# Performance work log

Measured on AMD Instinct MI355X. Metric: run time of the kernel, lower is better.

The kernel has to match this reference:

```python
import jax, jax.numpy as jnp
import numpy as np

N_MODEL = 1024
N_HEADS = 16
KV_HEADS = 4
HEAD_DIM = N_MODEL // N_HEADS          # 64
KV_MODEL = HEAD_DIM * KV_HEADS         # 256
GROUPS = N_HEADS // KV_HEADS           # 4
B, S = 4, 2048


def _rmsnorm(x):
    return x * jax.lax.rsqrt(jnp.mean(x * x, axis=-1, keepdims=True) + 1e-6)


def _act_quant(x):
    # 8-bit absmax per-token quantization (BitNet b1.58)
    scale = 127.0 / jnp.clip(jnp.max(jnp.abs(x), axis=-1, keepdims=True), 1e-5)
    return jnp.clip(jnp.round(x * scale), -128.0, 127.0) / scale


def _weight_quant(w):
    # ternary absmean quantization
    scale = 1.0 / jnp.clip(jnp.mean(jnp.abs(w)), 1e-5)
    return jnp.clip(jnp.round(w * scale), -1.0, 1.0) / scale


def bitlinear(x, w, b):
    xn = _rmsnorm(x)
    xq = xn + jax.lax.stop_gradient(_act_quant(xn) - xn)   # STE
    wq = w + jax.lax.stop_gradient(_weight_quant(w) - w)   # STE
    return jnp.einsum('...i,oi->...o', xq, wq) + b


def setup_inputs() -> dict:
    key = jax.random.key(0)
    ks = jax.random.split(key, 11)
    sq = 1.0 / np.sqrt(N_MODEL)
    sk = 1.0 / np.sqrt(KV_MODEL)
    return {
        'query': jax.random.normal(ks[0], (B, S, N_MODEL), jnp.float32),
        'key':   jax.random.normal(ks[1], (B, S, N_MODEL), jnp.float32),
        'value': jax.random.normal(ks[2], (B, S, N_MODEL), jnp.float32),
        'Wq': jax.random.normal(ks[3], (N_MODEL, N_MODEL), jnp.float32) * sq,
        'bq': jnp.zeros((N_MODEL,), jnp.float32),
        'Wk': jax.random.normal(ks[4], (KV_MODEL, N_MODEL), jnp.float32) * sq,
        'bk': jnp.zeros((KV_MODEL,), jnp.float32),
        'Wv': jax.random.normal(ks[5], (KV_MODEL, N_MODEL), jnp.float32) * sq,
        'bv': jnp.zeros((KV_MODEL,), jnp.float32),
        'Wo': jax.random.normal(ks[6], (N_MODEL, KV_MODEL), jnp.float32) * sk,
        'bo': jnp.zeros((N_MODEL,), jnp.float32),
    }


def reference(query, key, value, Wq, bq, Wk, bk, Wv, bv, Wo, bo):
    b = query.shape[0]
    Q = bitlinear(query, Wq, bq)   # [b, n, n_model]
    K = bitlinear(key,   Wk, bk)   # [b, s, kv_model]
    V = bitlinear(value, Wv, bv)   # [b, s, kv_model]

    # [b, h, n, d] layouts
    Q = Q.reshape(b, -1, N_HEADS, HEAD_DIM).transpose(0, 2, 1, 3)
    K = K.reshape(b, -1, KV_HEADS, HEAD_DIM).transpose(0, 2, 1, 3)
    V = V.reshape(b, -1, KV_HEADS, HEAD_DIM).transpose(0, 2, 1, 3)

    # group query heads: [b, g, kv_h, n, d]
    Qg = Q.reshape(b, KV_HEADS, GROUPS, -1, HEAD_DIM).transpose(0, 2, 1, 3, 4)
    # NOTE: faithful to the module, the einsum output has no 'g' axis,
    # so the grouped query heads are SUMMED over g.
    energy = jnp.einsum('bghnd,bhsd->bhns', Qg, K)  # [b, kv_h, n, s]

    scale = jnp.sqrt(jnp.float32(HEAD_DIM))
    attention = jax.nn.softmax(energy / scale, axis=-1)
    x = jnp.einsum('bhns,bhsd->bhnd', attention, V)  # [b, kv_h, n, d]
    x = x.transpose(0, 2, 1, 3).reshape(b, -1, KV_MODEL)
    x = bitlinear(x, Wo, bo)       # [b, n, n_model]
    return (x, attention)
```

## Files before the change

### kernel.cpp

```cpp
#include <hip/hip_runtime.h>
#include <stdint.h>

#define N_MODELC 1024
#define KV_MODELC 256
#define BATCH 4
#define SEQ 2048
#define NTOK (BATCH*SEQ)

typedef __attribute__((ext_vector_type(4))) float f32x4;
typedef __attribute__((ext_vector_type(4))) int   i32x4;
typedef __attribute__((ext_vector_type(8))) short s16x8;
typedef __attribute__((ext_vector_type(4))) short s16x4;

#define LOG2E 1.4426950408889634f
#define PSHIFT 32.0f

__device__ __forceinline__ unsigned short f2bf(float f){
  unsigned u = __builtin_bit_cast(unsigned, f);
  u = (u + 0x7FFFu + ((u>>16)&1u)) >> 16;
  return (unsigned short)u;
}
__device__ __forceinline__ float bf2f(unsigned short b){
  return __builtin_bit_cast(float, ((unsigned)b)<<16);
}

__global__ __launch_bounds__(256) void k_actquant1024(
    const float* __restrict__ xq_in, const float* __restrict__ xk_in, const float* __restrict__ xv_in,
    int8_t* __restrict__ q8q, int8_t* __restrict__ q8k, int8_t* __restrict__ q8v,
    float* __restrict__ scq, float* __restrict__ sck, float* __restrict__ scv)
{
  int row = blockIdx.x, which = blockIdx.y, t = threadIdx.x;
  const float* x = (which==0)?xq_in:(which==1)?xk_in:xv_in;
  int8_t* q8 = (which==0)?q8q:(which==1)?q8k:q8v;
  float* sc = (which==0)?scq:(which==1)?sck:scv;
  const float* xr = x + (size_t)row*N_MODELC;
  float4 v = reinterpret_cast<const float4*>(xr)[t];
  float ss = v.x*v.x + v.y*v.y + v.z*v.z + v.w*v.w;
  float am = fmaxf(fmaxf(fabsf(v.x),fabsf(v.y)), fmaxf(fabsf(v.z),fabsf(v.w)));
  #pragma unroll
  for (int m=32;m;m>>=1){ ss += __shfl_xor(ss,m,64); am = fmaxf(am, __shfl_xor(am,m,64)); }
  __shared__ float red[8];
  int wid = t>>6;
  if ((t&63)==0){ red[wid]=ss; red[4+wid]=am; }
  __syncthreads();
  ss = red[0]+red[1]+red[2]+red[3];
  am = fmaxf(fmaxf(red[4],red[5]), fmaxf(red[6],red[7]));
  float rinv = rsqrtf(ss*(1.0f/N_MODELC) + 1e-6f);
  float clipv = fmaxf(am*rinv, 1e-5f);
  float qs = 127.0f/clipv;
  float fsc = rinv*qs;
  char4 o;
  o.x = (signed char)(int)fminf(127.f, fmaxf(-128.f, rintf(v.x*fsc)));
  o.y = (signed char)(int)fminf(127.f, fmaxf(-128.f, rintf(v.y*fsc)));
  o.z = (signed char)(int)fminf(127.f, fmaxf(-128.f, rintf(v.z*fsc)));
  o.w = (signed char)(int)fminf(127.f, fmaxf(-128.f, rintf(v.w*fsc)));
  reinterpret_cast<char4*>(q8 + (size_t)row*N_MODELC)[t] = o;
  if (t==0) sc[row] = clipv*(1.0f/127.0f);
}

__global__ __launch_bounds__(64) void k_actquant256(
    const float* __restrict__ X, int8_t* __restrict__ q8, float* __restrict__ sc)
{
  int row = blockIdx.x, l = threadIdx.x;
  float4 v = reinterpret_cast<const float4*>(X + (size_t)row*KV_MODELC)[l];
  float ss = v.x*v.x + v.y*v.y + v.z*v.z + v.w*v.w;
  float am = fmaxf(fmaxf(fabsf(v.x),fabsf(v.y)), fmaxf(fabsf(v.z),fabsf(v.w)));
  #pragma unroll
  for (int m=32;m;m>>=1){ ss += __shfl_xor(ss,m,64); am = fmaxf(am, __shfl_xor(am,m,64)); }
  float rinv = rsqrtf(ss*(1.0f/KV_MODELC) + 1e-6f);
  float clipv = fmaxf(am*rinv, 1e-5f);
  float qs = 127.0f/clipv;
  float fsc = rinv*qs;
  char4 o;
  o.x = (signed char)(int)fminf(127.f, fmaxf(-128.f, rintf(v.x*fsc)));
  o.y = (signed char)(int)fminf(127.f, fmaxf(-128.f, rintf(v.y*fsc)));
  o.z = (signed char)(int)fminf(127.f, fmaxf(-128.f, rintf(v.z*fsc)));
  o.w = (signed char)(int)fminf(127.f, fmaxf(-128.f, rintf(v.w*fsc)));
  reinterpret_cast<char4*>(q8 + (size_t)row*KV_MODELC)[l] = o;
  if (l==0) sc[row] = clipv*(1.0f/127.0f);
}

__global__ __launch_bounds__(256) void k_wabs_partial(
    const float* __restrict__ Wq, const float* __restrict__ Wk,
    const float* __restrict__ Wv, const float* __restrict__ Wo, float* __restrict__ partial)
{
  int mat = blockIdx.y;
  const float* w = (mat==0)?Wq:(mat==1)?Wk:(mat==2)?Wv:Wo;
  int n = (mat==0)?(N_MODELC*N_MODELC):(KV_MODELC*N_MODELC);
  float s = 0.f;
  for (int i = blockIdx.x*256 + threadIdx.x; i < n; i += 256*256) s += fabsf(w[i]);
  #pragma unroll
  for (int m=32;m;m>>=1) s += __shfl_xor(s,m,64);
  __shared__ float red[4];
  int wid = threadIdx.x>>6;
  if ((threadIdx.x&63)==0) red[wid]=s;
  __syncthreads();
  if (threadIdx.x==0) partial[mat*256 + blockIdx.x] = red[0]+red[1]+red[2]+red[3];
}

__global__ __launch_bounds__(256) void k_wfinal(const float* __restrict__ partial, float* __restrict__ wfac)
{
  int mat = blockIdx.x, t = threadIdx.x;
  float s = partial[mat*256 + t];
  #pragma unroll
  for (int m=32;m;m>>=1) s += __shfl_xor(s,m,64);
  __shared__ float red[4];
  int wid = t>>6;
  if ((t&63)==0) red[wid]=s;
  __syncthreads();
  if (t==0){
    float tot = red[0]+red[1]+red[2]+red[3];
    float n = (mat==0)?(float)(N_MODELC*N_MODELC):(float)(KV_MODELC*N_MODELC);
    wfac[mat] = fmaxf(tot/n, 1e-5f);
  }
}

__global__ __launch_bounds__(256) void k_tern(
    const float* __restrict__ Wq, const float* __restrict__ Wk,
    const float* __restrict__ Wv, const float* __restrict__ Wo,
    const float* __restrict__ wfac,
    int8_t* __restrict__ Wqs, int8_t* __restrict__ Wkt,
    int8_t* __restrict__ Wvt, int8_t* __restrict__ Wot)
{
  int mat = blockIdx.y;
  int idx = blockIdx.x*256 + threadIdx.x;
  if (mat==0){
    float s = 1.0f/wfac[0];
    int op = idx>>10, i = idx&1023;
    int kv = op>>6, d = op&63;
    int acc = 0;
    #pragma unroll
    for (int g=0; g<4; g++){
      float w = Wq[(size_t)(kv*256 + g*64 + d)*N_MODELC + i];
      float r = fminf(1.f, fmaxf(-1.f, rintf(w*s)));
      acc += (int)r;
    }
    Wqs[idx] = (int8_t)acc;
  } else {
    const float* w = (mat==1)?Wk:(mat==2)?Wv:Wo;
    int8_t* o = (mat==1)?Wkt:(mat==2)?Wvt:Wot;
    float s = 1.0f/wfac[mat];
    float r = fminf(1.f, fmaxf(-1.f, rintf(w[idx]*s)));
    o[idx] = (int8_t)r;
  }
}

template<int MODE>
__global__ __launch_bounds__(512) void k_gemm_i8_1024(
    const int8_t* __restrict__ A, const int8_t* __restrict__ B,
    const float* __restrict__ rowscale, const float* __restrict__ wfac, int wfi,
    const float* __restrict__ bias, unsigned short* __restrict__ outp)
{
  __shared__ i32x4 redk[4][4][64];
  __shared__ unsigned short tlds[(MODE==2)?64:1][72];
  const int KDIM = 1024;
  int mb = blockIdx.x*64, nb = blockIdx.y*64;
  int w = threadIdx.x>>6, l = threadIdx.x&63, lr = l&15, lk = l>>4;
  int rw = w&3, kh = w>>2;
  const int8_t* Ap = A + (size_t)(mb + rw*16 + lr)*KDIM + kh*512 + lk*16;
  const int8_t* Bp = B + (size_t)(nb + lr)*KDIM + kh*512 + lk*16;
  i32x4 acc[4];
  #pragma unroll
  for (int f=0; f<4; f++) acc[f] = i32x4{0,0,0,0};
  #pragma unroll 4
  for (int kk=0; kk<512; kk+=64){
    i32x4 a = *reinterpret_cast<const i32x4*>(Ap + kk);
    #pragma unroll
    for (int f=0; f<4; f++){
      i32x4 b = *reinterpret_cast<const i32x4*>(Bp + (size_t)f*16*KDIM + kk);
      acc[f] = __builtin_amdgcn_mfma_i32_16x16x64_i8(a, b, acc[f], 0, 0, 0);
    }
  }
  if (kh==1){
    #pragma unroll
    for (int f=0; f<4; f++) redk[rw][f][l] = acc[f];
  }
  __syncthreads();
  if (kh==0){
    float wf = wfac[wfi];
    #pragma unroll
    for (int f=0; f<4; f++){
      acc[f] += redk[rw][f][l];
      int col = nb + f*16 + lr;
      float bval;
      if constexpr (MODE==0){
        int kv = col>>6, d = col&63;
        const float* bb = bias + kv*256 + d;
        bval = bb[0]+bb[64]+bb[128]+bb[192];
      } else {
        bval = bias[col];
      }
      #pragma unroll
      for (int r=0; r<4; r++){
        int row = mb + rw*16 + lk*4 + r;
        float val = (float)acc[f][r] * (rowscale[row]*wf) + bval;
        if constexpr (MODE==0){
          int bb2 = row>>11, s = row&2047, kvh = col>>6, d = col&63;
          outp[(((size_t)(bb2*4+kvh))*SEQ + s)*64 + d] = f2bf(0.125f*val);
        } else if constexpr (MODE==1){
          int bb2 = row>>11, s = row&2047, kvh = col>>6, d = col&63;
          outp[(((size_t)(bb2*4+kvh))*SEQ + s)*64 + d] = f2bf(val);
        } else {
          tlds[f*16+lr][rw*16 + lk*4 + r] = f2bf(val);
        }
      }
    }
  }
  if constexpr (MODE==2){
    __syncthreads();
    int u = threadIdx.x;
    int col = u>>3, part = u&7;
    int b = mb>>11, s0 = mb&2047;
    int bkv = b*4 + blockIdx.y, sT = s0>>6;
    s16x8 vv = *reinterpret_cast<const s16x8*>(&tlds[col][part*8]);
    *reinterpret_cast<s16x8*>(
        &outp[(((size_t)(bkv*32 + sT))*64 + col)*64 + part*8]) = vv;
  }
}

__global__ __launch_bounds__(256) void k_gemm_o(
    const int8_t* __restrict__ A, const int8_t* __restrict__ B,
    const float* __restrict__ rowscale, const float* __restrict__ wfac,
    const float* __restrict__ bias, float* __restrict__ outp)
{
  const int KDIM = 256;
  int mb = blockIdx.x*64, nb = blockIdx.y*64;
  int w = threadIdx.x>>6, l = threadIdx.x&63, lr = l&15, lk = l>>4;
  const int8_t* Ap = A + (size_t)(mb + w*16 + lr)*KDIM + lk*16;
  const int8_t* Bp = B + (size_t)(nb + lr)*KDIM + lk*16;
  i32x4 acc[4];
  #pragma unroll
  for (int f=0; f<4; f++) acc[f] = i32x4{0,0,0,0};
  #pragma unroll
  for (int kk=0; kk<KDIM; kk+=64){
    i32x4 a = *reinterpret_cast<const i32x4*>(Ap + kk);
    #pragma unroll
    for (int f=0; f<4; f++){
      i32x4 b = *reinterpret_cast<const i32x4*>(Bp + (size_t)f*16*KDIM + kk);
      acc[f] = __builtin_amdgcn_mfma_i32_16x16x64_i8(a, b, acc[f], 0, 0, 0);
    }
  }
  float wf = wfac[3];
  #pragma unroll
  for (int f=0; f<4; f++){
    int col = nb + f*16 + lr;
    float bval = bias[col];
    #pragma unroll
    for (int r=0; r<4; r++){
      int row = mb + w*16 + lk*4 + r;
      outp[(size_t)row*N_MODELC + col] = (float)acc[f][r]*(rowscale[row]*wf) + bval;
    }
  }
}

__global__ __launch_bounds__(128) void k_attn_full(
    const unsigned short* __restrict__ Qh, const unsigned short* __restrict__ Kh,
    const unsigned short* __restrict__ Vh,
    float* __restrict__ attn, float* __restrict__ X)
{
  __shared__ unsigned short plds[2][16][64];
  int bkv = blockIdx.y, b = bkv>>2, kv = bkv&3;
  int w = threadIdx.x>>6, l = threadIdx.x&63, lr = l&15, lk = l>>4;
  int rowt = blockIdx.x*32 + w*16;
  size_t tq = ((size_t)bkv*SEQ + rowt + lr)*64 + lk*8;
  s16x8 qa0 = *reinterpret_cast<const s16x8*>(Qh + tq);
  s16x8 qa1 = *reinterpret_cast<const s16x8*>(Qh + tq + 32);
  const unsigned short* kbase = Kh + (size_t)bkv*SEQ*64 + lk*8;
  const unsigned short* vbase = Vh + (size_t)bkv*32*4096 + lk*8;

  s16x8 ones;
  #pragma unroll
  for (int i=0;i<8;i++) ones[i] = (short)0x3F80;

  f32x4 acco[4];
  #pragma unroll
  for (int dt=0; dt<4; dt++) acco[dt] = f32x4{0.f,0.f,0.f,0.f};
  f32x4 accl = {0.f,0.f,0.f,0.f};

  int qwl = lk*4;
  int rswl = (lr&7)<<3;

  for (int st=0; st<SEQ; st+=64){
    #pragma unroll
    for (int sub=0; sub<4; sub++){
      int s0 = st + sub*16;
      const unsigned short* kp = kbase + (size_t)(s0+lr)*64;
      s16x8 k0 = *reinterpret_cast<const s16x8*>(kp);
      s16x8 k1 = *reinterpret_cast<const s16x8*>(kp + 32);
      f32x4 acc = {0.f,0.f,0.f,0.f};
      acc = __builtin_amdgcn_mfma_f32_16x16x32_bf16(qa0, k0, acc, 0,0,0);
      acc = __builtin_amdgcn_mfma_f32_16x16x32_bf16(qa1, k1, acc, 0,0,0);
      int slocal = sub*16 + lr;
      #pragma unroll
      for (int r=0;r<4;r++){
        float p = __builtin_amdgcn_exp2f(fmaf(acc[r], LOG2E, -PSHIFT));
        int sw = (slocal & 7) | ((((slocal>>3) ^ ((qwl+r)&7)))<<3);
        plds[w][qwl + r][sw] = f2bf(p);
      }
    }
    s16x8 a0 = *reinterpret_cast<const s16x8*>(&plds[w][lr][(lk<<3) ^ rswl]);
    s16x8 a1 = *reinterpret_cast<const s16x8*>(&plds[w][lr][((4+lk)<<3) ^ rswl]);
    accl = __builtin_amdgcn_mfma_f32_16x16x32_bf16(a0, ones, accl, 0,0,0);
    accl = __builtin_amdgcn_mfma_f32_16x16x32_bf16(a1, ones, accl, 0,0,0);
    const unsigned short* vt = vbase + (size_t)(st>>6)*4096;
    #pragma unroll
    for (int dt=0; dt<4; dt++){
      const unsigned short* vp = vt + (size_t)(dt*16+lr)*64;
      s16x8 b0 = *reinterpret_cast<const s16x8*>(vp);
      s16x8 b1 = *reinterpret_cast<const s16x8*>(vp + 32);
      acco[dt] = __builtin_amdgcn_mfma_f32_16x16x32_bf16(a0, b0, acco[dt], 0,0,0);
      acco[dt] = __builtin_amdgcn_mfma_f32_16x16x32_bf16(a1, b1, acco[dt], 0,0,0);
    }
  }

  float invr[4];
  #pragma unroll
  for (int r=0;r<4;r++) invr[r] = 1.0f/accl[r];
  int token = b*SEQ + rowt + qwl;
  #pragma unroll
  for (int dt=0; dt<4; dt++){
    #pragma unroll
    for (int r=0; r<4; r++){
      X[(size_t)(token + r)*KV_MODELC + kv*64 + dt*16 + lr] = acco[dt][r]*invr[r];
    }
  }

  float* arow = attn + (size_t)bkv*SEQ*SEQ + (size_t)rowt*SEQ;
  for (int st=0; st<SEQ; st+=64){
    #pragma unroll
    for (int sub=0; sub<4; sub++){
      int s0 = st + sub*16;
      const unsigned short* kp = kbase + (size_t)(s0+lr)*64;
      s16x8 k0 = *reinterpret_cast<const s16x8*>(kp);
      s16x8 k1 = *reinterpret_cast<const s16x8*>(kp + 32);
      f32x4 acc = {0.f,0.f,0.f,0.f};
      acc = __builtin_amdgcn_mfma_f32_16x16x32_bf16(qa0, k0, acc, 0,0,0);
      acc = __builtin_amdgcn_mfma_f32_16x16x32_bf16(qa1, k1, acc, 0,0,0);
      int slocal = sub*16 + lr;
      #pragma unroll
      for (int r=0;r<4;r++){
        float p = __builtin_amdgcn_exp2f(fmaf(acc[r], LOG2E, -PSHIFT))*invr[r];
        int sw = (slocal & 7) | ((((slocal>>3) ^ ((qwl+r)&7)))<<3);
        plds[w][qwl + r][sw] = f2bf(p);
      }
    }
    #pragma unroll
    for (int j=0; j<4; j++){
      int rowl = j*4 + (l>>4);
      int sseg = l & 15;
      int chunk = sseg >> 1, half = sseg & 1;
      int off = ((chunk ^ (rowl&7)) << 3) + (half<<2);
      s16x4 pb = *reinterpret_cast<const s16x4*>(&plds[w][rowl][off]);
      float4 o;
      o.x = bf2f((unsigned short)pb[0]);
      o.y = bf2f((unsigned short)pb[1]);
      o.z = bf2f((unsigned short)pb[2]);
      o.w = bf2f((unsigned short)pb[3]);
      *reinterpret_cast<float4*>(&arow[(size_t)rowl*SEQ + st + sseg*4]) = o;
    }
  }
}

extern "C" void kernel_launch(void* const* d_in, const int* in_sizes, int n_in,
                              void* d_out, int out_size, void* d_ws, size_t ws_size,
                              hipStream_t stream)
{
  (void)in_sizes; (void)n_in; (void)out_size; (void)ws_size;
  const float* q  = (const float*)d_in[0];
  const float* k  = (const float*)d_in[1];
  const float* v  = (const float*)d_in[2];
  const float* Wq = (const float*)d_in[3];
  const float* bq = (const float*)d_in[4];
  const float* Wk = (const float*)d_in[5];
  const float* bk = (const float*)d_in[6];
  const float* Wv = (const float*)d_in[7];
  const float* bv = (const float*)d_in[8];
  const float* Wo = (const float*)d_in[9];
  const float* bo = (const float*)d_in[10];

  float* out_x = (float*)d_out;
  float* out_attn = out_x + (size_t)NTOK*N_MODELC;

  char* ws = (char*)d_ws;
  size_t off = 0;
  auto alloc = [&](size_t bytes)->void*{
    void* p = ws + off; off += (bytes + 255) & ~(size_t)255; return p;
  };
  int8_t* q8q = (int8_t*)alloc((size_t)NTOK*N_MODELC);
  int8_t* q8k = (int8_t*)alloc((size_t)NTOK*N_MODELC);
  int8_t* q8v = (int8_t*)alloc((size_t)NTOK*N_MODELC);
  int8_t* q8x = (int8_t*)alloc((size_t)NTOK*KV_MODELC);
  float* scq = (float*)alloc(NTOK*4);
  float* sck = (float*)alloc(NTOK*4);
  float* scv = (float*)alloc(NTOK*4);
  float* scx = (float*)alloc(NTOK*4);
  float* partial = (float*)alloc(4*256*4);
  float* wfac = (float*)alloc(256);
  int8_t* Wqs = (int8_t*)alloc(256*1024);
  int8_t* Wkt = (int8_t*)alloc(256*1024);
  int8_t* Wvt = (int8_t*)alloc(256*1024);
  int8_t* Wot = (int8_t*)alloc(1024*256);
  unsigned short* Qh = (unsigned short*)alloc((size_t)NTOK*KV_MODELC*2);
  unsigned short* Kh = (unsigned short*)alloc((size_t)NTOK*KV_MODELC*2);
  unsigned short* Vh = (unsigned short*)alloc((size_t)NTOK*KV_MODELC*2);
  float* X = (float*)alloc((size_t)NTOK*KV_MODELC*4);

  hipLaunchKernelGGL(k_actquant1024, dim3(NTOK,3), dim3(256), 0, stream,
                     q,k,v, q8q,q8k,q8v, scq,sck,scv);
  hipLaunchKernelGGL(k_wabs_partial, dim3(256,4), dim3(256), 0, stream, Wq,Wk,Wv,Wo, partial);
  hipLaunchKernelGGL(k_wfinal, dim3(4), dim3(256), 0, stream, partial, wfac);
  hipLaunchKernelGGL(k_tern, dim3(1024,4), dim3(256), 0, stream,
                     Wq,Wk,Wv,Wo, wfac, Wqs,Wkt,Wvt,Wot);
  hipLaunchKernelGGL((k_gemm_i8_1024<0>), dim3(128,4), dim3(512), 0, stream,
                     q8q, Wqs, scq, wfac, 0, bq, Qh);
  hipLaunchKernelGGL((k_gemm_i8_1024<1>), dim3(128,4), dim3(512), 0, stream,
                     q8k, Wkt, sck, wfac, 1, bk, Kh);
  hipLaunchKernelGGL((k_gemm_i8_1024<2>), dim3(128,4), dim3(512), 0, stream,
                     q8v, Wvt, scv, wfac, 2, bv, Vh);
  hipLaunchKernelGGL(k_attn_full, dim3(64,16), dim3(128), 0, stream,
                     Qh, Kh, Vh, out_attn, X);
  hipLaunchKernelGGL(k_actquant256, dim3(NTOK), dim3(64), 0, stream, X, q8x, scx);
  hipLaunchKernelGGL(k_gemm_o, dim3(128,16), dim3(256), 0, stream,
                     q8x, Wot, scx, wfac, bo, out_x);
}
```

Before: 319.8 us.

## Split attention over sequence chunks with separate row-sum and PV reduction kernels

```diff
diff --git a/kernel.cpp b/kernel.cpp
--- a/kernel.cpp
+++ b/kernel.cpp
@@ -6,6 +6,8 @@
 #define BATCH 4
 #define SEQ 2048
 #define NTOK (BATCH*SEQ)
+#define NZ 4
+#define SCHUNK (SEQ/NZ)
 
 typedef __attribute__((ext_vector_type(4))) float f32x4;
 typedef __attribute__((ext_vector_type(4))) int   i32x4;
@@ -253,13 +255,59 @@
   }
 }
 
-__global__ __launch_bounds__(128) void k_attn_full(
+__global__ __launch_bounds__(128) void k_lsum(
     const unsigned short* __restrict__ Qh, const unsigned short* __restrict__ Kh,
-    const unsigned short* __restrict__ Vh,
-    float* __restrict__ attn, float* __restrict__ X)
+    float* __restrict__ lpart)
+{
+  int bkv = blockIdx.y, z = blockIdx.z;
+  int w = threadIdx.x>>6, l = threadIdx.x&63, lr = l&15, lk = l>>4;
+  int rowt = blockIdx.x*32 + w*16;
+  size_t tq = ((size_t)bkv*SEQ + rowt + lr)*64 + lk*8;
+  s16x8 qa0 = *reinterpret_cast<const s16x8*>(Qh + tq);
+  s16x8 qa1 = *reinterpret_cast<const s16x8*>(Qh + tq + 32);
+  const unsigned short* kbase = Kh + (size_t)bkv*SEQ*64 + lk*8;
+  float lsum[4] = {0.f,0.f,0.f,0.f};
+  for (int s0=z*SCHUNK; s0<z*SCHUNK+SCHUNK; s0+=16){
+    const unsigned short* kp = kbase + (size_t)(s0+lr)*64;
+    s16x8 k0 = *reinterpret_cast<const s16x8*>(kp);
+    s16x8 k1 = *reinterpret_cast<const s16x8*>(kp + 32);
+    f32x4 acc = {0.f,0.f,0.f,0.f};
+    acc = __builtin_amdgcn_mfma_f32_16x16x32_bf16(qa0, k0, acc, 0,0,0);
+    acc = __builtin_amdgcn_mfma_f32_16x16x32_bf16(qa1, k1, acc, 0,0,0);
+    #pragma unroll
+    for (int r=0;r<4;r++)
+      lsum[r] += __builtin_amdgcn_exp2f(fmaf(acc[r], LOG2E, -PSHIFT));
+  }
+  #pragma unroll
+  for (int r=0;r<4;r++){
+    #pragma unroll
+    for (int mask=1; mask<16; mask<<=1)
+      lsum[r] += __shfl_xor(lsum[r], mask, 64);
+  }
+  if (lr==0){
+    #pragma unroll
+    for (int r=0;r<4;r++)
+      lpart[((size_t)z*16 + bkv)*SEQ + rowt + lk*4 + r] = lsum[r];
+  }
+}
+
+__global__ __launch_bounds__(256) void k_linv(
+    const float* __restrict__ lpart, float* __restrict__ invl)
+{
+  int idx = blockIdx.x*256 + threadIdx.x;
+  float s = 0.f;
+  #pragma unroll
+  for (int z=0; z<NZ; z++) s += lpart[(size_t)z*16*SEQ + idx];
+  invl[idx] = 1.0f/s;
+}
+
+__global__ __launch_bounds__(128) void k_attn_pv2(
+    const unsigned short* __restrict__ Qh, const unsigned short* __restrict__ Kh,
+    const unsigned short* __restrict__ Vh, const float* __restrict__ invl,
+    float* __restrict__ attn, float* __restrict__ pvpart)
 {
   __shared__ unsigned short plds[2][16][64];
-  int bkv = blockIdx.y, b = bkv>>2, kv = bkv&3;
+  int bkv = blockIdx.y, z = blockIdx.z;
   int w = threadIdx.x>>6, l = threadIdx.x&63, lr = l&15, lk = l>>4;
   int rowt = blockIdx.x*32 + w*16;
   size_t tq = ((size_t)bkv*SEQ + rowt + lr)*64 + lk*8;
@@ -268,65 +316,19 @@
   const unsigned short* kbase = Kh + (size_t)bkv*SEQ*64 + lk*8;
   const unsigned short* vbase = Vh + (size_t)bkv*32*4096 + lk*8;
 
-  s16x8 ones;
-  #pragma unroll
-  for (int i=0;i<8;i++) ones[i] = (short)0x3F80;
+  float invr[4];
+  #pragma unroll
+  for (int r=0;r<4;r++) invr[r] = invl[(size_t)bkv*SEQ + rowt + lk*4 + r];
 
   f32x4 acco[4];
   #pragma unroll
   for (int dt=0; dt<4; dt++) acco[dt] = f32x4{0.f,0.f,0.f,0.f};
-  f32x4 accl = {0.f,0.f,0.f,0.f};
 
   int qwl = lk*4;
   int rswl = (lr&7)<<3;
-
-  for (int st=0; st<SEQ; st+=64){
-    #pragma unroll
-    for (int sub=0; sub<4; sub++){
-      int s0 = st + sub*16;
-      const unsigned short* kp = kbase + (size_t)(s0+lr)*64;
-      s16x8 k0 = *reinterpret_cast<const s16x8*>(kp);
-      s16x8 k1 = *reinterpret_cast<const s16x8*>(kp + 32);
-      f32x4 acc = {0.f,0.f,0.f,0.f};
-      acc = __builtin_amdgcn_mfma_f32_16x16x32_bf16(qa0, k0, acc, 0,0,0);
-      acc = __builtin_amdgcn_mfma_f32_16x16x32_bf16(qa1, k1, acc, 0,0,0);
-      int slocal = sub*16 + lr;
-      #pragma unroll
-      for (int r=0;r<4;r++){
-        float p = __builtin_amdgcn_exp2f(fmaf(acc[r], LOG2E, -PSHIFT));
-        int sw = (slocal & 7) | ((((slocal>>3) ^ ((qwl+r)&7)))<<3);
-        plds[w][qwl + r][sw] = f2bf(p);
-      }
-    }
-    s16x8 a0 = *reinterpret_cast<const s16x8*>(&plds[w][lr][(lk<<3) ^ rswl]);
-    s16x8 a1 = *reinterpret_cast<const s16x8*>(&plds[w][lr][((4+lk)<<3) ^ rswl]);
-    accl = __builtin_amdgcn_mfma_f32_16x16x32_bf16(a0, ones, accl, 0,0,0);
-    accl = __builtin_amdgcn_mfma_f32_16x16x32_bf16(a1, ones, accl, 0,0,0);
-    const unsigned short* vt = vbase + (size_t)(st>>6)*4096;
-    #pragma unroll
-    for (int dt=0; dt<4; dt++){
-      const unsigned short* vp = vt + (size_t)(dt*16+lr)*64;
-      s16x8 b0 = *reinterpret_cast<const s16x8*>(vp);
-      s16x8 b1 = *reinterpret_cast<const s16x8*>(vp + 32);
-      acco[dt] = __builtin_amdgcn_mfma_f32_16x16x32_bf16(a0, b0, acco[dt], 0,0,0);
-      acco[dt] = __builtin_amdgcn_mfma_f32_16x16x32_bf16(a1, b1, acco[dt], 0,0,0);
-    }
-  }
-
-  float invr[4];
-  #pragma unroll
-  for (int r=0;r<4;r++) invr[r] = 1.0f/accl[r];
-  int token = b*SEQ + rowt + qwl;
-  #pragma unroll
-  for (int dt=0; dt<4; dt++){
-    #pragma unroll
-    for (int r=0; r<4; r++){
-      X[(size_t)(token + r)*KV_MODELC + kv*64 + dt*16 + lr] = acco[dt][r]*invr[r];
-    }
-  }
-
   float* arow = attn + (size_t)bkv*SEQ*SEQ + (size_t)rowt*SEQ;
-  for (int st=0; st<SEQ; st+=64){
+
+  for (int st=z*SCHUNK; st<z*SCHUNK+SCHUNK; st+=64){
     #pragma unroll
     for (int sub=0; sub<4; sub++){
       int s0 = st + sub*16;
@@ -344,6 +346,17 @@
         plds[w][qwl + r][sw] = f2bf(p);
       }
     }
+    s16x8 a0 = *reinterpret_cast<const s16x8*>(&plds[w][lr][(lk<<3) ^ rswl]);
+    s16x8 a1 = *reinterpret_cast<const s16x8*>(&plds[w][lr][((4+lk)<<3) ^ rswl]);
+    const unsigned short* vt = vbase + (size_t)(st>>6)*4096;
+    #pragma unroll
+    for (int dt=0; dt<4; dt++){
+      const unsigned short* vp = vt + (size_t)(dt*16+lr)*64;
+      s16x8 b0 = *reinterpret_cast<const s16x8*>(vp);
+      s16x8 b1 = *reinterpret_cast<const s16x8*>(vp + 32);
+      acco[dt] = __builtin_amdgcn_mfma_f32_16x16x32_bf16(a0, b0, acco[dt], 0,0,0);
+      acco[dt] = __builtin_amdgcn_mfma_f32_16x16x32_bf16(a1, b1, acco[dt], 0,0,0);
+    }
     #pragma unroll
     for (int j=0; j<4; j++){
       int rowl = j*4 + (l>>4);
@@ -359,6 +372,36 @@
       *reinterpret_cast<float4*>(&arow[(size_t)rowl*SEQ + st + sseg*4]) = o;
     }
   }
+  float* base = pvpart + (((size_t)z*16 + bkv)*128 + blockIdx.x*2 + w)*1024;
+  #pragma unroll
+  for (int dt=0; dt<4; dt++)
+    *reinterpret_cast<f32x4*>(base + (dt*64 + l)*4) = acco[dt];
+}
+
+__global__ __launch_bounds__(256) void k_pvred(
+    const float* __restrict__ pvpart, float* __restrict__ X)
+{
+  __shared__ float xls[16][65];
+  int T = blockIdx.x;
+  int wt = T & 127, bkv = T>>7;
+  int b = bkv>>2, kv = bkv&3;
+  int t = threadIdx.x, l = t&63, dt = t>>6, lk = l>>4, lr = l&15;
+  f32x4 s = {0.f,0.f,0.f,0.f};
+  #pragma unroll
+  for (int z=0; z<NZ; z++){
+    f32x4 v = *reinterpret_cast<const f32x4*>(
+        pvpart + (((size_t)z*16 + bkv)*128 + wt)*1024 + t*4);
+    s += v;
+  }
+  #pragma unroll
+  for (int r=0; r<4; r++) xls[lk*4+r][dt*16+lr] = s[r];
+  __syncthreads();
+  int row = t>>4, col4 = (t&15)*4;
+  float4 o;
+  o.x = xls[row][col4];   o.y = xls[row][col4+1];
+  o.z = xls[row][col4+2]; o.w = xls[row][col4+3];
+  *reinterpret_cast<float4*>(
+      &X[((size_t)(b*SEQ + wt*16 + row))*KV_MODELC + kv*64 + col4]) = o;
 }
 
 extern "C" void kernel_launch(void* const* d_in, const int* in_sizes, int n_in,
@@ -404,6 +447,9 @@
   unsigned short* Kh = (unsigned short*)alloc((size_t)NTOK*KV_MODELC*2);
   unsigned short* Vh = (unsigned short*)alloc((size_t)NTOK*KV_MODELC*2);
   float* X = (float*)alloc((size_t)NTOK*KV_MODELC*4);
+  float* lpart = (float*)alloc((size_t)NZ*16*SEQ*4);
+  float* invl  = (float*)alloc((size_t)16*SEQ*4);
+  float* pvpart = (float*)alloc((size_t)NZ*16*128*1024*4);
 
   hipLaunchKernelGGL(k_actquant1024, dim3(NTOK,3), dim3(256), 0, stream,
                      q,k,v, q8q,q8k,q8v, scq,sck,scv);
@@ -417,8 +463,11 @@
                      q8k, Wkt, sck, wfac, 1, bk, Kh);
   hipLaunchKernelGGL((k_gemm_i8_1024<2>), dim3(128,4), dim3(512), 0, stream,
                      q8v, Wvt, scv, wfac, 2, bv, Vh);
-  hipLaunchKernelGGL(k_attn_full, dim3(64,16), dim3(128), 0, stream,
-                     Qh, Kh, Vh, out_attn, X);
+  hipLaunchKernelGGL(k_lsum, dim3(64,16,NZ), dim3(128), 0, stream, Qh, Kh, lpart);
+  hipLaunchKernelGGL(k_linv, dim3(16*SEQ/256), dim3(256), 0, stream, lpart, invl);
+  hipLaunchKernelGGL(k_attn_pv2, dim3(64,16,NZ), dim3(128), 0, stream,
+                     Qh, Kh, Vh, invl, out_attn, pvpart);
+  hipLaunchKernelGGL(k_pvred, dim3(2048), dim3(256), 0, stream, pvpart, X);
   hipLaunchKernelGGL(k_actquant256, dim3(NTOK), dim3(64), 0, stream, X, q8x, scx);
   hipLaunchKernelGGL(k_gemm_o, dim3(128,16), dim3(256), 0, stream,
                      q8x, Wot, scx, wfac, bo, out_x);
```

After: 334.9 us. +4.7%, slower.
